# Kernel tuning notes

Hardware: AMD Instinct MI355X
Metric: run time of the kernel (lower is better)

Reference implementation:

```python
import jax, jax.numpy as jnp
import numpy as np
import math

N, CIN, DM, H, W = 4, 64, 32, 64, 64
KH = KW = 3

def setup_inputs() -> dict:
    key = jax.random.key(0)
    ks = jax.random.split(key, 12)
    sc = 0.05
    return {
        "h": jax.random.normal(ks[0], (N, CIN, H, W), jnp.float32),
        "m": jax.random.normal(ks[1], (N, CIN, H, W), jnp.float32),
        "Wh": jax.random.normal(ks[2], (3 * DM, CIN), jnp.float32) * sc,
        "bh": jax.random.normal(ks[3], (3 * DM,), jnp.float32) * sc,
        "Wm": jax.random.normal(ks[4], (2 * DM, CIN), jnp.float32) * sc,
        "bm": jax.random.normal(ks[5], (2 * DM,), jnp.float32) * sc,
        "Wz": jax.random.normal(ks[6], (DM, 2 * DM), jnp.float32) * sc,
        "bz": jax.random.normal(ks[7], (DM,), jnp.float32) * sc,
        "Wo": jax.random.normal(ks[8], (3 * CIN, CIN + DM, KH, KW), jnp.float32) * sc,
        "bo": jax.random.normal(ks[9], (3 * CIN,), jnp.float32) * sc,
    }

def _conv1x1(x, Wt, b):
    # x: [N,Ci,H,W], Wt: [Co,Ci] -> [N,Co,H,W]
    return jnp.einsum('oi,nihw->nohw', Wt, x) + b[None, :, None, None]

def _attend(q, k, v):
    # q,k,v: [N,C,S]; out: [N,C,S]
    C = q.shape[1]
    scores = jnp.einsum('ncs,nct->nst', q, k) / math.sqrt(C)  # [N,S,S]
    attn = jax.nn.softmax(scores, axis=-1)
    return jnp.einsum('nst,nct->ncs', attn, v)

def reference(h, m, Wh, bh, Wm, bm, Wz, bz, Wo, bo):
    n, _, hh, ww = h.shape
    S = hh * ww
    hq, hk, hv = jnp.split(_conv1x1(h, Wh, bh), 3, axis=1)
    mk, mv = jnp.split(_conv1x1(m, Wm, bm), 2, axis=1)
    hq = hq.reshape(n, DM, S)
    hk = hk.reshape(n, DM, S)
    hv = hv.reshape(n, DM, S)
    mk = mk.reshape(n, DM, S)
    mv = mv.reshape(n, DM, S)
    Zh = _attend(hq, hk, hv).reshape(n, DM, hh, ww)
    Zm = _attend(hq, mk, mv).reshape(n, DM, hh, ww)
    Z = _conv1x1(jnp.concatenate([Zh, Zm], axis=1), Wz, bz)
    x = jnp.concatenate([Z, h], axis=1)  # [N, DM+CIN, H, W]
    out = jax.lax.conv_general_dilated(
        x, Wo, window_strides=(1, 1), padding='SAME',
        dimension_numbers=('NCHW', 'OIHW', 'NCHW')) + bo[None, :, None, None]
    i, g, o = jnp.split(out, 3, axis=1)
    i = jax.nn.sigmoid(i)
    g = jnp.tanh(g)
    m_next = i * g + (1.0 - i) * m
    h_next = jax.nn.sigmoid(o) * m_next
    return (h_next, m_next)
```

## Files before the change

### kernel.cpp

```cpp
#include <hip/hip_runtime.h>
#include <math.h>

#define NB 4
#define CIN 64
#define DM 32
#define S 4096
#define NW 4

#define OFF_Q  0
#define OFF_KH 262144
#define OFF_VH 524288
#define OFF_KM 786432
#define OFF_VM 1048576
#define OFF_ZH 1310720
#define OFF_ZM 1572864
#define OFF_WF 1835008

typedef __attribute__((ext_vector_type(8))) short bf16x8;
typedef __attribute__((ext_vector_type(4))) short s16x4;
typedef __attribute__((ext_vector_type(4))) float f32x4;
typedef __attribute__((ext_vector_type(2))) unsigned int u32x2;

__device__ inline unsigned short f2b(float x) {
  union { float f; unsigned u; } v;
  v.f = x;
  unsigned r = (v.u + 0x7FFF + ((v.u >> 16) & 1)) >> 16;
  return (unsigned short)r;
}

__device__ inline float b2f(unsigned short u) {
  union { unsigned u; float f; } v;
  v.u = ((unsigned)u) << 16;
  return v.f;
}

__device__ inline unsigned fbits(float x) {
  union { float f; unsigned u; } v;
  v.f = x;
  return v.u;
}

__global__ __launch_bounds__(256) void prep_kernel(
    const float* __restrict__ h, const float* __restrict__ m,
    const float* __restrict__ Wh, const float* __restrict__ bh,
    const float* __restrict__ Wm, const float* __restrict__ bm,
    const float* __restrict__ Wo, float* __restrict__ ws) {
  __shared__ unsigned short sm[64][34];
  int bid = blockIdx.x;
  int tid = threadIdx.x;

  if (bid >= 512) {
    int idx = (bid - 512) * 256 + tid;
    int co = idx / 432;
    int rem = idx - co * 432;
    int tap = rem / 48;
    int cp = rem - tap * 48;
    int ci0 = cp * 2;
    float a = Wo[((size_t)co * 96 + ci0) * 9 + tap];
    float b = Wo[((size_t)co * 96 + ci0 + 1) * 9 + tap];
    unsigned val = (unsigned)f2b(a) | ((unsigned)f2b(b) << 16);
    ((unsigned*)(ws + OFF_WF))[idx] = val;
    return;
  }

  int mode = (bid >= 256) ? 1 : 0;
  const float* in = mode ? m : h;
  const float* W = mode ? Wm : Wh;
  const float* b = mode ? bm : bh;
  int lbid = bid & 255;
  int n = lbid >> 6;
  int s0 = (lbid & 63) * 64;
  int sl = tid & 63;
  int cg = tid >> 6;
  const float* inp = in + (size_t)n * CIN * S + s0 + sl;

  float reg[64];
#pragma unroll
  for (int ci = 0; ci < 64; ++ci) reg[ci] = inp[(size_t)ci * S];

  float acc[24];
  if (mode == 0) {
#pragma unroll
    for (int k = 0; k < 24; ++k) {
      int co = cg + k * 4;
      const float* w = W + co * CIN;
      float a = b[co];
#pragma unroll
      for (int ci = 0; ci < CIN; ++ci) a += w[ci] * reg[ci];
      acc[k] = a;
    }
  } else {
#pragma unroll
    for (int k = 0; k < 16; ++k) {
      int co = cg + k * 4;
      const float* w = W + co * CIN;
      float a = b[co];
#pragma unroll
      for (int ci = 0; ci < CIN; ++ci) a += w[ci] * reg[ci];
      acc[k] = a;
    }
  }

  unsigned short* qsl = (unsigned short*)(ws + OFF_Q);
  unsigned short* khs = (unsigned short*)(ws + OFF_KH);
  unsigned short* vhs = (unsigned short*)(ws + OFF_VH);
  unsigned short* kms = (unsigned short*)(ws + OFF_KM);
  unsigned short* vms = (unsigned short*)(ws + OFF_VM);

  int ngrp = (mode == 0) ? 2 : 1;
  for (int g = 0; g < ngrp; ++g) {
    __syncthreads();
    const float rs = 0.2550400330665387f;
#pragma unroll
    for (int j = 0; j < 8; ++j) {
      int k = g * 8 + j;
      int c = cg + 4 * j;
      float v = acc[k];
      if (mode == 0 && g == 0) v *= rs;
      sm[sl][c] = f2b(v);
    }
    __syncthreads();
    unsigned short* dst;
    if (mode == 0)
      dst = (g == 0 ? qsl : khs);
    else
      dst = kms;
    unsigned* du = (unsigned*)(dst + ((size_t)n * S + s0) * 32);
#pragma unroll
    for (int i = 0; i < 4; ++i) {
      int idx = tid + i * 256;
      int s = idx >> 4, cp = idx & 15;
      unsigned val = (unsigned)sm[s][2 * cp] | ((unsigned)sm[s][2 * cp + 1] << 16);
      du[idx] = val;
    }
  }
  int k0 = (mode == 0) ? 16 : 8;
  unsigned short* vdst = (mode == 0) ? vhs : vms;
#pragma unroll
  for (int j = 0; j < 8; ++j) {
    int k = k0 + j;
    int c = cg + 4 * j;
    vdst[((size_t)n * DM + c) * S + s0 + sl] = f2b(acc[k]);
  }
}

union AttnSmem {
  unsigned short P[NW][2][1240];
  float osh[NW][2][32][16];
};

__global__ __launch_bounds__(256, 4) void attn_kernel(
    float* __restrict__ ws, const float* __restrict__ Wz,
    const float* __restrict__ bz) {
  __shared__ AttnSmem sm;
  __shared__ float lsh[NW][2][16];
  __shared__ unsigned short Olds[2][16][40];

  int bid = blockIdx.x;
  int ph = bid & 1;
  int n = (bid >> 1) & 3;
  int q0 = (bid >> 3) * 32;
  int tid = threadIdx.x;
  int w = tid >> 6;
  int lane = tid & 63;
  int ql = lane & 15;
  int quad = lane >> 4;
  int kbase = w * 1024;

  const unsigned short* qs = (const unsigned short*)(ws + OFF_Q) + ((size_t)n * S + q0) * 32;
  const unsigned short* Ks = (const unsigned short*)(ws + (ph ? OFF_KM : OFF_KH)) + (size_t)n * S * 32;
  const unsigned short* Vs = (const unsigned short*)(ws + (ph ? OFF_VM : OFF_VH)) + (size_t)n * DM * S;
  unsigned short* Zp = (unsigned short*)(ws + (ph ? OFF_ZM : OFF_ZH)) + (size_t)n * DM * S;

  bf16x8 qf0 = *(const bf16x8*)(qs + ql * 32 + quad * 8);
  bf16x8 qf1 = *(const bf16x8*)(qs + (16 + ql) * 32 + quad * 8);

  f32x4 o00 = {0.f, 0.f, 0.f, 0.f}, o01 = {0.f, 0.f, 0.f, 0.f};
  f32x4 o10 = {0.f, 0.f, 0.f, 0.f}, o11 = {0.f, 0.f, 0.f, 0.f};
  f32x4 lsv0 = {0.f, 0.f, 0.f, 0.f}, lsv1 = {0.f, 0.f, 0.f, 0.f};
  const float ZI = -11.541560327111707f;
  const f32x4 zinit = {ZI, ZI, ZI, ZI};

  bf16x8 kf[4], kfn[4], vf[4];
#pragma unroll
  for (int t = 0; t < 4; ++t)
    kf[t] = *(const bf16x8*)(Ks + (size_t)(kbase + t * 16 + ql) * 32 + quad * 8);

  for (int it = 0; it < 16; ++it) {
    int kb = kbase + it * 64;
    int kbn = kbase + ((it + 1) & 15) * 64;
#pragma unroll
    for (int c2 = 0; c2 < 2; ++c2)
#pragma unroll
      for (int t2 = 0; t2 < 2; ++t2)
        vf[c2 * 2 + t2] = *(const bf16x8*)(Vs + (size_t)(t2 * 16 + ql) * S + kb + c2 * 32 + quad * 8);
#pragma unroll
    for (int t = 0; t < 4; ++t)
      kfn[t] = *(const bf16x8*)(Ks + (size_t)(kbn + t * 16 + ql) * 32 + quad * 8);

#pragma unroll
    for (int t = 0; t < 4; ++t) {
      f32x4 stt = __builtin_amdgcn_mfma_f32_16x16x32_bf16(kf[t], qf0, zinit, 0, 0, 0);
      f32x4 e;
#pragma unroll
      for (int r = 0; r < 4; ++r) e[r] = __builtin_amdgcn_exp2f(stt[r]);
      lsv0 += e;
      u32x2 pk;
      pk[0] = __builtin_amdgcn_perm(fbits(e[1]), fbits(e[0]), 0x07060302u);
      pk[1] = __builtin_amdgcn_perm(fbits(e[3]), fbits(e[2]), 0x07060302u);
      *(u32x2*)(&sm.P[w][0][ql * 76 + t * 16 + quad * 4]) = pk;
    }
#pragma unroll
    for (int t = 0; t < 4; ++t) {
      f32x4 stt = __builtin_amdgcn_mfma_f32_16x16x32_bf16(kf[t], qf1, zinit, 0, 0, 0);
      f32x4 e;
#pragma unroll
      for (int r = 0; r < 4; ++r) e[r] = __builtin_amdgcn_exp2f(stt[r]);
      lsv1 += e;
      u32x2 pk;
      pk[0] = __builtin_amdgcn_perm(fbits(e[1]), fbits(e[0]), 0x07060302u);
      pk[1] = __builtin_amdgcn_perm(fbits(e[3]), fbits(e[2]), 0x07060302u);
      *(u32x2*)(&sm.P[w][1][ql * 76 + t * 16 + quad * 4]) = pk;
    }

    __builtin_amdgcn_s_waitcnt(0xC07F);
    __builtin_amdgcn_wave_barrier();

#pragma unroll
    for (int c2 = 0; c2 < 2; ++c2) {
      bf16x8 pf0 = *(const bf16x8*)(&sm.P[w][0][ql * 76 + c2 * 32 + quad * 8]);
      bf16x8 pf1 = *(const bf16x8*)(&sm.P[w][1][ql * 76 + c2 * 32 + quad * 8]);
      o00 = __builtin_amdgcn_mfma_f32_16x16x32_bf16(vf[c2 * 2 + 0], pf0, o00, 0, 0, 0);
      o01 = __builtin_amdgcn_mfma_f32_16x16x32_bf16(vf[c2 * 2 + 1], pf0, o01, 0, 0, 0);
      o10 = __builtin_amdgcn_mfma_f32_16x16x32_bf16(vf[c2 * 2 + 0], pf1, o10, 0, 0, 0);
      o11 = __builtin_amdgcn_mfma_f32_16x16x32_bf16(vf[c2 * 2 + 1], pf1, o11, 0, 0, 0);
    }
    __builtin_amdgcn_wave_barrier();

#pragma unroll
    for (int t = 0; t < 4; ++t) kf[t] = kfn[t];
  }

  float lrun0 = lsv0[0] + lsv0[1] + lsv0[2] + lsv0[3];
  float lrun1 = lsv1[0] + lsv1[1] + lsv1[2] + lsv1[3];
  lrun0 += __shfl_xor(lrun0, 16);
  lrun0 += __shfl_xor(lrun0, 32);
  lrun1 += __shfl_xor(lrun1, 16);
  lrun1 += __shfl_xor(lrun1, 32);

  __syncthreads();
#pragma unroll
  for (int r = 0; r < 4; ++r) {
    sm.osh[w][0][quad * 4 + r][ql] = o00[r];
    sm.osh[w][0][16 + quad * 4 + r][ql] = o01[r];
    sm.osh[w][1][quad * 4 + r][ql] = o10[r];
    sm.osh[w][1][16 + quad * 4 + r][ql] = o11[r];
  }
  if (quad == 0) {
    lsh[w][0][ql] = lrun0;
    lsh[w][1][ql] = lrun1;
  }
  __syncthreads();

  if (w < 2) {
    int qt = w;
    float l = 0.f;
    f32x4 a0 = {0.f, 0.f, 0.f, 0.f}, a1 = {0.f, 0.f, 0.f, 0.f};
#pragma unroll
    for (int i = 0; i < NW; ++i) {
      l += lsh[i][qt][ql];
#pragma unroll
      for (int r = 0; r < 4; ++r) {
        a0[r] += sm.osh[i][qt][quad * 4 + r][ql];
        a1[r] += sm.osh[i][qt][16 + quad * 4 + r][ql];
      }
    }
    float inv = 1.0f / l;
    s16x4 w0, w1;
#pragma unroll
    for (int r = 0; r < 4; ++r) {
      w0[r] = (short)f2b(a0[r] * inv);
      w1[r] = (short)f2b(a1[r] * inv);
    }
    *(s16x4*)(&Olds[qt][ql][quad * 4]) = w0;
    *(s16x4*)(&Olds[qt][ql][16 + quad * 4]) = w1;
    __builtin_amdgcn_s_waitcnt(0xC07F);
    __builtin_amdgcn_wave_barrier();
    bf16x8 of = *(const bf16x8*)(&Olds[qt][ql][quad * 8]);

    const float* wzr0 = Wz + (size_t)ql * (2 * DM) + ph * DM + quad * 8;
    const float* wzr1 = Wz + (size_t)(ql + 16) * (2 * DM) + ph * DM + quad * 8;
    bf16x8 a0f, a1f;
#pragma unroll
    for (int j = 0; j < 8; ++j) {
      a0f[j] = (short)f2b(wzr0[j]);
      a1f[j] = (short)f2b(wzr1[j]);
    }
    f32x4 z0 = {0.f, 0.f, 0.f, 0.f}, z1 = {0.f, 0.f, 0.f, 0.f};
    if (ph == 0) {
#pragma unroll
      for (int r = 0; r < 4; ++r) {
        z0[r] = bz[quad * 4 + r];
        z1[r] = bz[16 + quad * 4 + r];
      }
    }
    z0 = __builtin_amdgcn_mfma_f32_16x16x32_bf16(a0f, of, z0, 0, 0, 0);
    z1 = __builtin_amdgcn_mfma_f32_16x16x32_bf16(a1f, of, z1, 0, 0, 0);
    int qc = q0 + qt * 16 + ql;
#pragma unroll
    for (int r = 0; r < 4; ++r) {
      Zp[(size_t)(quad * 4 + r) * S + qc] = f2b(z0[r]);
      Zp[(size_t)(16 + quad * 4 + r) * S + qc] = f2b(z1[r]);
    }
  }
}

__global__ __launch_bounds__(256) void xsfill_kernel(
    float* __restrict__ ws, const float* __restrict__ h) {
  __shared__ float lin[96][65];
  int bid = blockIdx.x;
  int n = bid >> 6, y = bid & 63;
  int tid = threadIdx.x;
  const unsigned short* Zh = (const unsigned short*)(ws + OFF_ZH) + (size_t)n * DM * S + y * 64;
  const unsigned short* Zm = (const unsigned short*)(ws + OFF_ZM) + (size_t)n * DM * S + y * 64;
  const float* hb = h + ((size_t)n * 64) * S + y * 64;
#pragma unroll
  for (int k = 0; k < 24; ++k) {
    int idx = tid + k * 256;
    int ci = idx >> 6, xx = idx & 63;
    float v;
    if (ci < 32)
      v = b2f(Zh[(size_t)ci * S + xx]) + b2f(Zm[(size_t)ci * S + xx]);
    else
      v = hb[((size_t)(ci - 32)) * S + xx];
    lin[ci][xx] = v;
  }
  __syncthreads();
  unsigned short* rowbase = (unsigned short*)ws + (((size_t)n * 66 + y + 1) * 66) * 96;
  unsigned* xrow = (unsigned*)(rowbase + 96);
#pragma unroll
  for (int k = 0; k < 12; ++k) {
    int u = tid + k * 256;
    int xx = u / 48, cp = u - xx * 48;
    unsigned val = (unsigned)f2b(lin[2 * cp][xx]) | ((unsigned)f2b(lin[2 * cp + 1][xx]) << 16);
    xrow[u] = val;
  }
  if (tid < 96) {
    if (tid < 48)
      ((unsigned*)rowbase)[tid] = 0u;
    else
      ((unsigned*)(rowbase + 65 * 96))[tid - 48] = 0u;
  }
  if (y == 0) {
    unsigned* g = (unsigned*)((unsigned short*)ws + ((size_t)n * 66) * 66 * 96);
    for (int k = 0; k < 13; ++k) {
      int idx = tid + k * 256;
      if (idx < 3168) g[idx] = 0u;
    }
  }
  if (y == 63) {
    unsigned* g = (unsigned*)((unsigned short*)ws + (((size_t)n * 66 + 65) * 66) * 96);
    for (int k = 0; k < 13; ++k) {
      int idx = tid + k * 256;
      if (idx < 3168) g[idx] = 0u;
    }
  }
}

__global__ __launch_bounds__(256) void conv_mfma_kernel(
    const float* __restrict__ ws, const float* __restrict__ m,
    const float* __restrict__ bo, float* __restrict__ out) {
  int bid = blockIdx.x;
  int n = bid >> 7;
  int rem = bid & 127;
  int g = rem & 1;
  int sblk = rem >> 1;
  int tid = threadIdx.x;
  int wv = tid >> 6;
  int lane = tid & 63;
  int ql = lane & 15, quad = lane >> 4;
  int s0 = sblk * 64 + wv * 16;
  int y = s0 >> 6, x0 = s0 & 63;

  const unsigned short* xs = (const unsigned short*)ws;
  const unsigned short* Wf = (const unsigned short*)(ws + OFF_WF);

  f32x4 acc[6];
#pragma unroll
  for (int t = 0; t < 6; ++t) acc[t] = (f32x4){0.f, 0.f, 0.f, 0.f};

  const unsigned short* xb = xs + (((size_t)n * 66 + y) * 66 + (x0 + ql)) * 96 + quad * 8;
  const unsigned short* wb[6];
#pragma unroll
  for (int j = 0; j < 6; ++j) {
    int cob = (j >> 1) * 64 + g * 32 + (j & 1) * 16;
    wb[j] = Wf + (size_t)(cob + ql) * 864 + quad * 8;
  }

#pragma unroll
  for (int dy = 0; dy < 3; ++dy) {
#pragma unroll
    for (int dx = 0; dx < 3; ++dx) {
      int tap = dy * 3 + dx;
      const unsigned short* xp = xb + ((size_t)dy * 66 + dx) * 96;
#pragma unroll
      for (int cc = 0; cc < 3; ++cc) {
        bf16x8 b = *(const bf16x8*)(xp + cc * 32);
        int ko = tap * 96 + cc * 32;
#pragma unroll
        for (int j = 0; j < 6; ++j) {
          bf16x8 wf = *(const bf16x8*)(wb[j] + ko);
          acc[j] = __builtin_amdgcn_mfma_f32_16x16x32_bf16(wf, b, acc[j], 0, 0, 0);
        }
      }
    }
  }

  int s = s0 + ql;
#pragma unroll
  for (int jj = 0; jj < 2; ++jj) {
#pragma unroll
    for (int r = 0; r < 4; ++r) {
      int c = g * 32 + jj * 16 + quad * 4 + r;
      float iv = acc[jj][r] + bo[c];
      float gv = acc[2 + jj][r] + bo[64 + c];
      float ov = acc[4 + jj][r] + bo[128 + c];
      float ig = 1.f / (1.f + __expf(-iv));
      float gg = tanhf(gv);
      float og = 1.f / (1.f + __expf(-ov));
      size_t oidx = (((size_t)n * 64 + c) << 12) + s;
      float mold = m[oidx];
      float mn = ig * gg + (1.f - ig) * mold;
      out[oidx] = og * mn;
      out[(size_t)NB * CIN * S + oidx] = mn;
    }
  }
}

extern "C" void kernel_launch(void* const* d_in, const int* in_sizes, int n_in,
                              void* d_out, int out_size, void* d_ws, size_t ws_size,
                              hipStream_t stream) {
  const float* h = (const float*)d_in[0];
  const float* m = (const float*)d_in[1];
  const float* Wh = (const float*)d_in[2];
  const float* bh = (const float*)d_in[3];
  const float* Wm = (const float*)d_in[4];
  const float* bm = (const float*)d_in[5];
  const float* Wz = (const float*)d_in[6];
  const float* bz = (const float*)d_in[7];
  const float* Wo = (const float*)d_in[8];
  const float* bo = (const float*)d_in[9];
  float* out = (float*)d_out;
  float* ws = (float*)d_ws;

  prep_kernel<<<836, 256, 0, stream>>>(h, m, Wh, bh, Wm, bm, Wo, ws);
  attn_kernel<<<2 * NB * (S / 32), 256, 0, stream>>>(ws, Wz, bz);
  xsfill_kernel<<<NB * 64, 256, 0, stream>>>(ws, h);
  conv_mfma_kernel<<<NB * 128, 256, 0, stream>>>(ws, m, bo, out);
}
```

Before: 186.5 us.

## Fuse xsfill into conv via shared-memory halo tile and swizzle attention P buffer

Removes the separate xsfill kernel. The conv kernel now builds its own 3-row padded bf16 input tile in shared memory, directly from Zh, Zm and h, which removes one launch and the padded global intermediate. The attention kernel switches its P scratch from a padded stride-76 layout to an XOR-swizzled stride-64 layout to avoid LDS bank conflicts. It also unrolls the K-prefetch loop by two with ping-pong registers to drop the register copies. The trade-off is that each conv block now recomputes Z sums for three rows, so Z is loaded about three times overall.

```diff
diff --git a/kernel.cpp b/kernel.cpp
--- a/kernel.cpp
+++ b/kernel.cpp
@@ -145,14 +145,14 @@
 }
 
 union AttnSmem {
-  unsigned short P[NW][2][1240];
+  unsigned short P[NW][2][1024];
   float osh[NW][2][32][16];
 };
 
 __global__ __launch_bounds__(256, 4) void attn_kernel(
     float* __restrict__ ws, const float* __restrict__ Wz,
     const float* __restrict__ bz) {
-  __shared__ AttnSmem sm;
+  __shared__ __align__(16) AttnSmem sm;
   __shared__ float lsh[NW][2][16];
   __shared__ unsigned short Olds[2][16][40];
 
@@ -166,6 +166,7 @@
   int ql = lane & 15;
   int quad = lane >> 4;
   int kbase = w * 1024;
+  int sw = 2 * (ql & 7);
 
   const unsigned short* qs = (const unsigned short*)(ws + OFF_Q) + ((size_t)n * S + q0) * 32;
   const unsigned short* Ks = (const unsigned short*)(ws + (ph ? OFF_KM : OFF_KH)) + (size_t)n * S * 32;
@@ -181,14 +182,13 @@
   const float ZI = -11.541560327111707f;
   const f32x4 zinit = {ZI, ZI, ZI, ZI};
 
-  bf16x8 kf[4], kfn[4], vf[4];
+  bf16x8 kfa[4], kfb[4];
 #pragma unroll
   for (int t = 0; t < 4; ++t)
-    kf[t] = *(const bf16x8*)(Ks + (size_t)(kbase + t * 16 + ql) * 32 + quad * 8);
-
-  for (int it = 0; it < 16; ++it) {
-    int kb = kbase + it * 64;
-    int kbn = kbase + ((it + 1) & 15) * 64;
+    kfa[t] = *(const bf16x8*)(Ks + (size_t)(kbase + t * 16 + ql) * 32 + quad * 8);
+
+  auto step = [&](bf16x8 (&kfc)[4], bf16x8 (&kfn)[4], int kb, int kbn) {
+    bf16x8 vf[4];
 #pragma unroll
     for (int c2 = 0; c2 < 2; ++c2)
 #pragma unroll
@@ -200,7 +200,7 @@
 
 #pragma unroll
     for (int t = 0; t < 4; ++t) {
-      f32x4 stt = __builtin_amdgcn_mfma_f32_16x16x32_bf16(kf[t], qf0, zinit, 0, 0, 0);
+      f32x4 stt = __builtin_amdgcn_mfma_f32_16x16x32_bf16(kfc[t], qf0, zinit, 0, 0, 0);
       f32x4 e;
 #pragma unroll
       for (int r = 0; r < 4; ++r) e[r] = __builtin_amdgcn_exp2f(stt[r]);
@@ -208,11 +208,11 @@
       u32x2 pk;
       pk[0] = __builtin_amdgcn_perm(fbits(e[1]), fbits(e[0]), 0x07060302u);
       pk[1] = __builtin_amdgcn_perm(fbits(e[3]), fbits(e[2]), 0x07060302u);
-      *(u32x2*)(&sm.P[w][0][ql * 76 + t * 16 + quad * 4]) = pk;
+      *(u32x2*)(&sm.P[w][0][ql * 64 + ((t * 4 + quad) ^ sw) * 4]) = pk;
     }
 #pragma unroll
     for (int t = 0; t < 4; ++t) {
-      f32x4 stt = __builtin_amdgcn_mfma_f32_16x16x32_bf16(kf[t], qf1, zinit, 0, 0, 0);
+      f32x4 stt = __builtin_amdgcn_mfma_f32_16x16x32_bf16(kfc[t], qf1, zinit, 0, 0, 0);
       f32x4 e;
 #pragma unroll
       for (int r = 0; r < 4; ++r) e[r] = __builtin_amdgcn_exp2f(stt[r]);
@@ -220,7 +220,7 @@
       u32x2 pk;
       pk[0] = __builtin_amdgcn_perm(fbits(e[1]), fbits(e[0]), 0x07060302u);
       pk[1] = __builtin_amdgcn_perm(fbits(e[3]), fbits(e[2]), 0x07060302u);
-      *(u32x2*)(&sm.P[w][1][ql * 76 + t * 16 + quad * 4]) = pk;
+      *(u32x2*)(&sm.P[w][1][ql * 64 + ((t * 4 + quad) ^ sw) * 4]) = pk;
     }
 
     __builtin_amdgcn_s_waitcnt(0xC07F);
@@ -228,17 +228,22 @@
 
 #pragma unroll
     for (int c2 = 0; c2 < 2; ++c2) {
-      bf16x8 pf0 = *(const bf16x8*)(&sm.P[w][0][ql * 76 + c2 * 32 + quad * 8]);
-      bf16x8 pf1 = *(const bf16x8*)(&sm.P[w][1][ql * 76 + c2 * 32 + quad * 8]);
+      bf16x8 pf0 = *(const bf16x8*)(&sm.P[w][0][ql * 64 + ((c2 * 8 + quad * 2) ^ sw) * 4]);
+      bf16x8 pf1 = *(const bf16x8*)(&sm.P[w][1][ql * 64 + ((c2 * 8 + quad * 2) ^ sw) * 4]);
       o00 = __builtin_amdgcn_mfma_f32_16x16x32_bf16(vf[c2 * 2 + 0], pf0, o00, 0, 0, 0);
       o01 = __builtin_amdgcn_mfma_f32_16x16x32_bf16(vf[c2 * 2 + 1], pf0, o01, 0, 0, 0);
       o10 = __builtin_amdgcn_mfma_f32_16x16x32_bf16(vf[c2 * 2 + 0], pf1, o10, 0, 0, 0);
       o11 = __builtin_amdgcn_mfma_f32_16x16x32_bf16(vf[c2 * 2 + 1], pf1, o11, 0, 0, 0);
     }
     __builtin_amdgcn_wave_barrier();
-
-#pragma unroll
-    for (int t = 0; t < 4; ++t) kf[t] = kfn[t];
+  };
+
+  for (int it = 0; it < 16; it += 2) {
+    int kb0 = kbase + it * 64;
+    int kb1 = kbase + ((it + 1) & 15) * 64;
+    int kb2 = kbase + ((it + 2) & 15) * 64;
+    step(kfa, kfb, kb0, kb1);
+    step(kfb, kfa, kb1, kb2);
   }
 
   float lrun0 = lsv0[0] + lsv0[1] + lsv0[2] + lsv0[3];
@@ -315,81 +320,68 @@
   }
 }
 
-__global__ __launch_bounds__(256) void xsfill_kernel(
-    float* __restrict__ ws, const float* __restrict__ h) {
-  __shared__ float lin[96][65];
-  int bid = blockIdx.x;
-  int n = bid >> 6, y = bid & 63;
-  int tid = threadIdx.x;
-  const unsigned short* Zh = (const unsigned short*)(ws + OFF_ZH) + (size_t)n * DM * S + y * 64;
-  const unsigned short* Zm = (const unsigned short*)(ws + OFF_ZM) + (size_t)n * DM * S + y * 64;
-  const float* hb = h + ((size_t)n * 64) * S + y * 64;
-#pragma unroll
-  for (int k = 0; k < 24; ++k) {
-    int idx = tid + k * 256;
-    int ci = idx >> 6, xx = idx & 63;
-    float v;
-    if (ci < 32)
-      v = b2f(Zh[(size_t)ci * S + xx]) + b2f(Zm[(size_t)ci * S + xx]);
-    else
-      v = hb[((size_t)(ci - 32)) * S + xx];
-    lin[ci][xx] = v;
-  }
-  __syncthreads();
-  unsigned short* rowbase = (unsigned short*)ws + (((size_t)n * 66 + y + 1) * 66) * 96;
-  unsigned* xrow = (unsigned*)(rowbase + 96);
-#pragma unroll
-  for (int k = 0; k < 12; ++k) {
-    int u = tid + k * 256;
-    int xx = u / 48, cp = u - xx * 48;
-    unsigned val = (unsigned)f2b(lin[2 * cp][xx]) | ((unsigned)f2b(lin[2 * cp + 1][xx]) << 16);
-    xrow[u] = val;
-  }
-  if (tid < 96) {
-    if (tid < 48)
-      ((unsigned*)rowbase)[tid] = 0u;
-    else
-      ((unsigned*)(rowbase + 65 * 96))[tid - 48] = 0u;
-  }
-  if (y == 0) {
-    unsigned* g = (unsigned*)((unsigned short*)ws + ((size_t)n * 66) * 66 * 96);
-    for (int k = 0; k < 13; ++k) {
-      int idx = tid + k * 256;
-      if (idx < 3168) g[idx] = 0u;
-    }
-  }
-  if (y == 63) {
-    unsigned* g = (unsigned*)((unsigned short*)ws + (((size_t)n * 66 + 65) * 66) * 96);
-    for (int k = 0; k < 13; ++k) {
-      int idx = tid + k * 256;
-      if (idx < 3168) g[idx] = 0u;
-    }
-  }
-}
-
 __global__ __launch_bounds__(256) void conv_mfma_kernel(
-    const float* __restrict__ ws, const float* __restrict__ m,
-    const float* __restrict__ bo, float* __restrict__ out) {
+    const float* __restrict__ ws, const float* __restrict__ h,
+    const float* __restrict__ m, const float* __restrict__ bo,
+    float* __restrict__ out) {
+  __shared__ unsigned short xt[3][66][104];
   int bid = blockIdx.x;
   int n = bid >> 7;
   int rem = bid & 127;
   int g = rem & 1;
-  int sblk = rem >> 1;
+  int y = rem >> 1;
   int tid = threadIdx.x;
   int wv = tid >> 6;
   int lane = tid & 63;
   int ql = lane & 15, quad = lane >> 4;
-  int s0 = sblk * 64 + wv * 16;
-  int y = s0 >> 6, x0 = s0 & 63;
-
-  const unsigned short* xs = (const unsigned short*)ws;
+  int x0 = wv * 16;
+
+  const unsigned short* Zh = (const unsigned short*)(ws + OFF_ZH) + (size_t)n * DM * S;
+  const unsigned short* Zm = (const unsigned short*)(ws + OFF_ZM) + (size_t)n * DM * S;
+  const float* hb = h + (size_t)n * CIN * S;
   const unsigned short* Wf = (const unsigned short*)(ws + OFF_WF);
 
+#pragma unroll
+  for (int k = 0; k < 36; ++k) {
+    int idx = tid + k * 256;
+    int xm1 = idx & 63;
+    int t2 = idx >> 6;
+    int cp = t2 % 48;
+    int r3 = t2 / 48;
+    int yy = y + r3 - 1;
+    unsigned val = 0u;
+    if (yy >= 0 && yy < 64) {
+      int s = yy * 64 + xm1;
+      int ci0 = 2 * cp;
+      float a, b;
+      if (ci0 < 32) {
+        a = b2f(Zh[(size_t)ci0 * S + s]) + b2f(Zm[(size_t)ci0 * S + s]);
+        b = b2f(Zh[(size_t)(ci0 + 1) * S + s]) + b2f(Zm[(size_t)(ci0 + 1) * S + s]);
+      } else {
+        a = hb[(size_t)(ci0 - 32) * S + s];
+        b = hb[(size_t)(ci0 - 31) * S + s];
+      }
+      val = (unsigned)f2b(a) | ((unsigned)f2b(b) << 16);
+    }
+    *(unsigned*)(&xt[r3][xm1 + 1][2 * cp]) = val;
+  }
+#pragma unroll
+  for (int k = 0; k < 2; ++k) {
+    int idx = tid + k * 256;
+    if (idx < 288) {
+      int r3 = idx / 96;
+      int rm = idx % 96;
+      int side = rm / 48;
+      int cp = rm % 48;
+      *(unsigned*)(&xt[r3][side * 65][2 * cp]) = 0u;
+    }
+  }
+  __syncthreads();
+
   f32x4 acc[6];
 #pragma unroll
   for (int t = 0; t < 6; ++t) acc[t] = (f32x4){0.f, 0.f, 0.f, 0.f};
 
-  const unsigned short* xb = xs + (((size_t)n * 66 + y) * 66 + (x0 + ql)) * 96 + quad * 8;
   const unsigned short* wb[6];
 #pragma unroll
   for (int j = 0; j < 6; ++j) {
@@ -402,10 +394,9 @@
 #pragma unroll
     for (int dx = 0; dx < 3; ++dx) {
       int tap = dy * 3 + dx;
-      const unsigned short* xp = xb + ((size_t)dy * 66 + dx) * 96;
 #pragma unroll
       for (int cc = 0; cc < 3; ++cc) {
-        bf16x8 b = *(const bf16x8*)(xp + cc * 32);
+        bf16x8 b = *(const bf16x8*)(&xt[dy][x0 + ql + dx][cc * 32 + quad * 8]);
         int ko = tap * 96 + cc * 32;
 #pragma unroll
         for (int j = 0; j < 6; ++j) {
@@ -416,7 +407,7 @@
     }
   }
 
-  int s = s0 + ql;
+  int s = y * 64 + x0 + ql;
 #pragma unroll
   for (int jj = 0; jj < 2; ++jj) {
 #pragma unroll
@@ -455,6 +446,5 @@
 
   prep_kernel<<<836, 256, 0, stream>>>(h, m, Wh, bh, Wm, bm, Wo, ws);
   attn_kernel<<<2 * NB * (S / 32), 256, 0, stream>>>(ws, Wz, bz);
-  xsfill_kernel<<<NB * 64, 256, 0, stream>>>(ws, h);
-  conv_mfma_kernel<<<NB * 128, 256, 0, stream>>>(ws, m, bo, out);
-}
+  conv_mfma_kernel<<<NB * 128, 256, 0, stream>>>(ws, h, m, bo, out);
+}
```

Measured after the change: 186.4 us. Within noise of the previous version (-0.0%).
